# Kernel tuning notes

Hardware: AMD Instinct MI355X
Metric: run time of the kernel (lower is better)

Reference implementation:

```python
import jax, jax.numpy as jnp
import numpy as np

B, S, DIM, DA = 64, 4096, 256, 64
NEG = -1e30

def setup_inputs() -> dict:
    key = jax.random.key(0)
    k1, k2, k3, k4 = jax.random.split(key, 4)
    h = jax.random.normal(k1, (B, S, DIM), dtype=jnp.float32)
    mask = jax.random.randint(k2, (B, S), 0, 2).astype(jnp.bool_)
    # xavier_uniform with gain=1.414 as in the torch module
    lim_a = 1.414 * np.sqrt(6.0 / (DIM + DA))
    lim_b = 1.414 * np.sqrt(6.0 / (DA + 1))
    a = jax.random.uniform(k3, (DIM, DA), minval=-lim_a, maxval=lim_a, dtype=jnp.float32)
    b = jax.random.uniform(k4, (DA, 1), minval=-lim_b, maxval=lim_b, dtype=jnp.float32)
    return {"h": h, "mask": mask, "a": a, "b": b}

def reference(h, mask, a, b):
    # e: (B, S) additive-attention logits
    e = jnp.einsum('bsk,ko->bs', jnp.tanh(jnp.einsum('bsd,dk->bsk', h, a)), b)
    e = e + mask.astype(e.dtype) * NEG  # True == padding -> -1e30
    attn = jax.nn.softmax(e, axis=1)    # softmax over seq dim
    # weighted sum over seq: (B, DIM)
    return jnp.einsum('bs,bsd->bd', attn, h)
```

## Files before the change

kernel.cpp:

```cpp
#include <hip/hip_runtime.h>
#include <hip/hip_bf16.h>

#define B_    64
#define S_    4096
#define DIM_  256
#define DA_   64
#define NEG_  (-1e30f)

typedef __attribute__((ext_vector_type(8))) short short8;
typedef __attribute__((ext_vector_type(4))) float float4v;

static __device__ inline unsigned short f2bf(float x) {
    union { float f; unsigned u; } v; v.f = x;
    unsigned r = v.u + 0x7fffu + ((v.u >> 16) & 1u);
    return (unsigned short)(r >> 16);
}

__global__ __launch_bounds__(256) void prep_kernel(
    const float* __restrict__ a, const void* __restrict__ mask,
    unsigned short* __restrict__ at_sw, int* __restrict__ flag)
{
    int idx = blockIdx.x * 256 + threadIdx.x;
    int j    = idx & 7;
    int lane = (idx >> 3) & 63;
    int kbnt = idx >> 9;
    int kb   = kbnt & 7;
    int nt   = kbnt >> 3;
    int d  = kb * 32 + (lane >> 4) * 8 + j;
    int kf = nt * 16 + (lane & 15);
    at_sw[idx] = f2bf(a[d * DA_ + kf]);

    if (blockIdx.x == 0) {
        __shared__ int anynz;
        if (threadIdx.x == 0) anynz = 0;
        __syncthreads();
        const unsigned char* mb = (const unsigned char*)mask;
        int base = threadIdx.x * 4;
        int v = mb[base + 1] | mb[base + 2] | mb[base + 3];
        if (v) atomicOr(&anynz, 1);
        __syncthreads();
        if (threadIdx.x == 0) *flag = (anynz == 0) ? 1 : 0;
    }
}

__global__ __launch_bounds__(256) void logits_kernel(
    const float* __restrict__ h, const unsigned short* __restrict__ at_sw,
    const float* __restrict__ bvec, float* __restrict__ e,
    unsigned short* __restrict__ h16)
{
    __shared__ unsigned short hs[64 * 264];
    const int t = threadIdx.x;
    const long long s0 = (long long)blockIdx.x * 64;
    const float* hblk = h + s0 * DIM_;
    unsigned short* h16blk = h16 + s0 * DIM_;

    #pragma unroll
    for (int j = 0; j < 8; ++j) {
        int f2 = t + j * 256;
        int row = f2 >> 5;
        int col = (f2 & 31) * 8;
        const float* src = hblk + row * DIM_ + col;
        float4 v0 = *(const float4*)(src);
        float4 v1 = *(const float4*)(src + 4);
        uint2 p0, p1;
        p0.x = f2bf(v0.x) | ((unsigned)f2bf(v0.y) << 16);
        p0.y = f2bf(v0.z) | ((unsigned)f2bf(v0.w) << 16);
        p1.x = f2bf(v1.x) | ((unsigned)f2bf(v1.y) << 16);
        p1.y = f2bf(v1.z) | ((unsigned)f2bf(v1.w) << 16);
        *(uint2*)&hs[row * 264 + col]     = p0;
        *(uint2*)&hs[row * 264 + col + 4] = p1;
        union { _Float16 hh[8]; uint4 u; } pk;
        pk.hh[0] = (_Float16)v0.x; pk.hh[1] = (_Float16)v0.y;
        pk.hh[2] = (_Float16)v0.z; pk.hh[3] = (_Float16)v0.w;
        pk.hh[4] = (_Float16)v1.x; pk.hh[5] = (_Float16)v1.y;
        pk.hh[6] = (_Float16)v1.z; pk.hh[7] = (_Float16)v1.w;
        *(uint4*)(h16blk + (size_t)f2 * 8) = pk.u;
    }
    __syncthreads();

    const int wave = t >> 6;
    const int lane = t & 63;
    const int quad = lane >> 4;
    const int nrow = lane & 15;

    float4v acc[4];
    #pragma unroll
    for (int nt = 0; nt < 4; ++nt) acc[nt] = (float4v){0.f, 0.f, 0.f, 0.f};

    const unsigned short* hrow = &hs[(wave * 16 + nrow) * 264];
    #pragma unroll
    for (int kb = 0; kb < 8; ++kb) {
        short8 afrag = *(const short8*)(hrow + kb * 32 + quad * 8);
        #pragma unroll
        for (int nt = 0; nt < 4; ++nt) {
            short8 bfrag = *(const short8*)(at_sw + ((nt * 8 + kb) * 64 + lane) * 8);
            acc[nt] = __builtin_amdgcn_mfma_f32_16x16x32_bf16(afrag, bfrag, acc[nt], 0, 0, 0);
        }
    }

    float bv[4];
    #pragma unroll
    for (int nt = 0; nt < 4; ++nt) bv[nt] = bvec[nt * 16 + nrow];

    #pragma unroll
    for (int r = 0; r < 4; ++r) {
        float p = 0.f;
        #pragma unroll
        for (int nt = 0; nt < 4; ++nt) p += tanhf(acc[nt][r]) * bv[nt];
        p += __shfl_xor(p, 1);
        p += __shfl_xor(p, 2);
        p += __shfl_xor(p, 4);
        p += __shfl_xor(p, 8);
        if (nrow == r)
            e[s0 + wave * 16 + quad * 4 + r] = p;
    }
}

__global__ __launch_bounds__(1024) void softmax_kernel(
    float* __restrict__ e, const void* __restrict__ mask, const int* __restrict__ flag)
{
    const int b = blockIdx.x;
    const int t = threadIdx.x;
    const bool int32enc = (*flag != 0);
    const long long base = (long long)b * S_;

    float ev[4];
    #pragma unroll
    for (int i = 0; i < 4; ++i) {
        int s = t + i * 1024;
        float x = e[base + s];
        int m;
        if (int32enc) m = ((const int*)mask)[base + s];
        else          m = ((const unsigned char*)mask)[base + s];
        ev[i] = m ? NEG_ : x;
    }

    __shared__ float red[16];
    float mx = fmaxf(fmaxf(ev[0], ev[1]), fmaxf(ev[2], ev[3]));
    #pragma unroll
    for (int off = 32; off >= 1; off >>= 1) mx = fmaxf(mx, __shfl_xor(mx, off));
    if ((t & 63) == 0) red[t >> 6] = mx;
    __syncthreads();
    float m = red[0];
    #pragma unroll
    for (int i = 1; i < 16; ++i) m = fmaxf(m, red[i]);
    __syncthreads();

    float ex[4];
    float l = 0.f;
    #pragma unroll
    for (int i = 0; i < 4; ++i) { ex[i] = __expf(ev[i] - m); l += ex[i]; }
    #pragma unroll
    for (int off = 32; off >= 1; off >>= 1) l += __shfl_xor(l, off);
    if ((t & 63) == 0) red[t >> 6] = l;
    __syncthreads();
    float lt = 0.f;
    #pragma unroll
    for (int i = 0; i < 16; ++i) lt += red[i];

    float inv = 1.0f / lt;
    #pragma unroll
    for (int i = 0; i < 4; ++i) e[base + t + i * 1024] = ex[i] * inv;
}

__global__ __launch_bounds__(256) void wsum_kernel(
    const unsigned short* __restrict__ h16, const float* __restrict__ w,
    float* __restrict__ out)
{
    const int b = blockIdx.x >> 3;
    const int c = blockIdx.x & 7;
    const int t = threadIdx.x;
    const int wv = t >> 6;
    const int col = (t & 63) * 4;

    __shared__ float wch[512];
    __shared__ float red[4 * 256];
    const int sbase = c * 512;
    wch[t]       = w[(long long)b * S_ + sbase + t];
    wch[t + 256] = w[(long long)b * S_ + sbase + t + 256];
    __syncthreads();

    const unsigned short* hb = h16 + ((long long)b * S_ + sbase) * DIM_;
    float a0 = 0.f, a1 = 0.f, a2 = 0.f, a3 = 0.f;
    #pragma unroll 4
    for (int i = 0; i < 128; ++i) {
        int s = i * 4 + wv;
        union { ushort4 u; _Float16 hh[4]; } pk;
        pk.u = *(const ushort4*)(hb + (size_t)s * DIM_ + col);
        float wt = wch[s];
        a0 = fmaf(wt, (float)pk.hh[0], a0);
        a1 = fmaf(wt, (float)pk.hh[1], a1);
        a2 = fmaf(wt, (float)pk.hh[2], a2);
        a3 = fmaf(wt, (float)pk.hh[3], a3);
    }
    red[wv * 256 + col + 0] = a0;
    red[wv * 256 + col + 1] = a1;
    red[wv * 256 + col + 2] = a2;
    red[wv * 256 + col + 3] = a3;
    __syncthreads();

    float sum = red[t] + red[256 + t] + red[512 + t] + red[768 + t];
    atomicAdd(&out[b * DIM_ + t], sum);
}

extern "C" void kernel_launch(void* const* d_in, const int* in_sizes, int n_in,
                              void* d_out, int out_size, void* d_ws, size_t ws_size,
                              hipStream_t stream) {
    const float* h    = (const float*)d_in[0];
    const void*  mask = d_in[1];
    const float* a    = (const float*)d_in[2];
    const float* bvec = (const float*)d_in[3];
    float* out = (float*)d_out;

    char* ws = (char*)d_ws;
    unsigned short* at_sw = (unsigned short*)ws;
    int* flag             = (int*)(ws + 32768);
    float* e              = (float*)(ws + 36864);
    unsigned short* h16   = (unsigned short*)(ws + 1085440);

    hipMemsetAsync(d_out, 0, (size_t)B_ * DIM_ * sizeof(float), stream);
    prep_kernel<<<64, 256, 0, stream>>>(a, mask, at_sw, flag);
    logits_kernel<<<(B_ * S_) / 64, 256, 0, stream>>>(h, at_sw, bvec, e, h16);
    softmax_kernel<<<B_, 1024, 0, stream>>>(e, mask, flag);
    wsum_kernel<<<B_ * 8, 256, 0, stream>>>(h16, e, out);
}
```

Before: 420.9 us.

## Fuse logits, online softmax and weighted sum into one chunked kernel

Replaces the separate logits, softmax and weighted-sum kernels with one kernel. Each block handles a 256-row chunk of one batch and keeps an online (flash-style) running max and sum, accumulating the weighted sum from the fp16 tile already held in shared memory. A small merge kernel then rescales and combines the per-chunk partials. This removes the fp16 copy of h written to and re-read from global memory, the logits round trip, the memset and the atomics. In exchange the grid drops to 1024 blocks with serialized tiles and no overlap between load and compute, and the MFMA now uses fp16 instead of bf16.

```diff
diff --git a/kernel.cpp b/kernel.cpp
--- a/kernel.cpp
+++ b/kernel.cpp
@@ -1,24 +1,23 @@
 #include <hip/hip_runtime.h>
 #include <hip/hip_bf16.h>
 
-#define B_    64
-#define S_    4096
-#define DIM_  256
-#define DA_   64
-#define NEG_  (-1e30f)
-
-typedef __attribute__((ext_vector_type(8))) short short8;
-typedef __attribute__((ext_vector_type(4))) float float4v;
-
-static __device__ inline unsigned short f2bf(float x) {
-    union { float f; unsigned u; } v; v.f = x;
-    unsigned r = v.u + 0x7fffu + ((v.u >> 16) & 1u);
-    return (unsigned short)(r >> 16);
-}
+#define B_      64
+#define S_      4096
+#define DIM_    256
+#define DA_     64
+#define NEG_    (-1e30f)
+#define CHUNKS_ 16
+#define ROWS_   256
+#define TILES_  4
+#define LDH_    264
+#define PSTR_   258
+
+typedef _Float16 half8 __attribute__((ext_vector_type(8)));
+typedef float float4v __attribute__((ext_vector_type(4)));
 
 __global__ __launch_bounds__(256) void prep_kernel(
     const float* __restrict__ a, const void* __restrict__ mask,
-    unsigned short* __restrict__ at_sw, int* __restrict__ flag)
+    _Float16* __restrict__ at_sw, int* __restrict__ flag)
 {
     int idx = blockIdx.x * 256 + threadIdx.x;
     int j    = idx & 7;
@@ -28,7 +27,7 @@
     int nt   = kbnt >> 3;
     int d  = kb * 32 + (lane >> 4) * 8 + j;
     int kf = nt * 16 + (lane & 15);
-    at_sw[idx] = f2bf(a[d * DA_ + kf]);
+    at_sw[idx] = (_Float16)a[d * DA_ + kf];
 
     if (blockIdx.x == 0) {
         __shared__ int anynz;
@@ -43,164 +42,149 @@
     }
 }
 
-__global__ __launch_bounds__(256) void logits_kernel(
-    const float* __restrict__ h, const unsigned short* __restrict__ at_sw,
-    const float* __restrict__ bvec, float* __restrict__ e,
-    unsigned short* __restrict__ h16)
+__global__ __launch_bounds__(256) void fused_kernel(
+    const float* __restrict__ h, const _Float16* __restrict__ at_sw,
+    const float* __restrict__ bvec, const void* __restrict__ mask,
+    const int* __restrict__ flag, float* __restrict__ part)
 {
-    __shared__ unsigned short hs[64 * 264];
+    __shared__ _Float16 hf[64 * LDH_];
+    __shared__ float e_l[64];
+    __shared__ float w_l[64];
+    __shared__ float red[4 * 256];
+    __shared__ float m_s, l_s, resc_s;
+
     const int t = threadIdx.x;
-    const long long s0 = (long long)blockIdx.x * 64;
-    const float* hblk = h + s0 * DIM_;
-    unsigned short* h16blk = h16 + s0 * DIM_;
-
-    #pragma unroll
-    for (int j = 0; j < 8; ++j) {
-        int f2 = t + j * 256;
-        int row = f2 >> 5;
-        int col = (f2 & 31) * 8;
-        const float* src = hblk + row * DIM_ + col;
-        float4 v0 = *(const float4*)(src);
-        float4 v1 = *(const float4*)(src + 4);
-        uint2 p0, p1;
-        p0.x = f2bf(v0.x) | ((unsigned)f2bf(v0.y) << 16);
-        p0.y = f2bf(v0.z) | ((unsigned)f2bf(v0.w) << 16);
-        p1.x = f2bf(v1.x) | ((unsigned)f2bf(v1.y) << 16);
-        p1.y = f2bf(v1.z) | ((unsigned)f2bf(v1.w) << 16);
-        *(uint2*)&hs[row * 264 + col]     = p0;
-        *(uint2*)&hs[row * 264 + col + 4] = p1;
-        union { _Float16 hh[8]; uint4 u; } pk;
-        pk.hh[0] = (_Float16)v0.x; pk.hh[1] = (_Float16)v0.y;
-        pk.hh[2] = (_Float16)v0.z; pk.hh[3] = (_Float16)v0.w;
-        pk.hh[4] = (_Float16)v1.x; pk.hh[5] = (_Float16)v1.y;
-        pk.hh[6] = (_Float16)v1.z; pk.hh[7] = (_Float16)v1.w;
-        *(uint4*)(h16blk + (size_t)f2 * 8) = pk.u;
-    }
-    __syncthreads();
-
+    const int b = blockIdx.x >> 4;
+    const int c = blockIdx.x & (CHUNKS_ - 1);
     const int wave = t >> 6;
     const int lane = t & 63;
     const int quad = lane >> 4;
     const int nrow = lane & 15;
-
-    float4v acc[4];
-    #pragma unroll
-    for (int nt = 0; nt < 4; ++nt) acc[nt] = (float4v){0.f, 0.f, 0.f, 0.f};
-
-    const unsigned short* hrow = &hs[(wave * 16 + nrow) * 264];
-    #pragma unroll
-    for (int kb = 0; kb < 8; ++kb) {
-        short8 afrag = *(const short8*)(hrow + kb * 32 + quad * 8);
-        #pragma unroll
-        for (int nt = 0; nt < 4; ++nt) {
-            short8 bfrag = *(const short8*)(at_sw + ((nt * 8 + kb) * 64 + lane) * 8);
-            acc[nt] = __builtin_amdgcn_mfma_f32_16x16x32_bf16(afrag, bfrag, acc[nt], 0, 0, 0);
-        }
-    }
-
+    const bool int32enc = (*flag != 0);
+
+    if (t == 0) { m_s = NEG_; l_s = 0.f; }
+
+    const float* hb = h + ((long long)b * S_ + c * ROWS_) * DIM_;
     float bv[4];
     #pragma unroll
     for (int nt = 0; nt < 4; ++nt) bv[nt] = bvec[nt * 16 + nrow];
 
-    #pragma unroll
-    for (int r = 0; r < 4; ++r) {
-        float p = 0.f;
-        #pragma unroll
-        for (int nt = 0; nt < 4; ++nt) p += tanhf(acc[nt][r]) * bv[nt];
-        p += __shfl_xor(p, 1);
-        p += __shfl_xor(p, 2);
-        p += __shfl_xor(p, 4);
-        p += __shfl_xor(p, 8);
-        if (nrow == r)
-            e[s0 + wave * 16 + quad * 4 + r] = p;
+    const int dbase = (t & 63) * 4;
+    float acc0 = 0.f, acc1 = 0.f, acc2 = 0.f, acc3 = 0.f;
+
+    for (int tile = 0; tile < TILES_; ++tile) {
+        const float* hsrc = hb + (size_t)tile * 64 * DIM_;
+        #pragma unroll
+        for (int j = 0; j < 8; ++j) {
+            int f2 = t + j * 256;
+            int row = f2 >> 5;
+            int col = (f2 & 31) * 8;
+            const float* src = hsrc + row * DIM_ + col;
+            float4 v0 = *(const float4*)(src);
+            float4 v1 = *(const float4*)(src + 4);
+            union { _Float16 hh[8]; uint4 u; } pk;
+            pk.hh[0] = (_Float16)v0.x; pk.hh[1] = (_Float16)v0.y;
+            pk.hh[2] = (_Float16)v0.z; pk.hh[3] = (_Float16)v0.w;
+            pk.hh[4] = (_Float16)v1.x; pk.hh[5] = (_Float16)v1.y;
+            pk.hh[6] = (_Float16)v1.z; pk.hh[7] = (_Float16)v1.w;
+            *(uint4*)&hf[row * LDH_ + col] = pk.u;
+        }
+        __syncthreads();
+
+        float4v accm[4];
+        #pragma unroll
+        for (int nt = 0; nt < 4; ++nt) accm[nt] = (float4v){0.f, 0.f, 0.f, 0.f};
+        const _Float16* hrow = &hf[(wave * 16 + nrow) * LDH_];
+        #pragma unroll
+        for (int kb = 0; kb < 8; ++kb) {
+            half8 af = *(const half8*)(hrow + kb * 32 + quad * 8);
+            #pragma unroll
+            for (int nt = 0; nt < 4; ++nt) {
+                half8 bf = *(const half8*)(at_sw + ((nt * 8 + kb) * 64 + lane) * 8);
+                accm[nt] = __builtin_amdgcn_mfma_f32_16x16x32_f16(af, bf, accm[nt], 0, 0, 0);
+            }
+        }
+        #pragma unroll
+        for (int r = 0; r < 4; ++r) {
+            float p = 0.f;
+            #pragma unroll
+            for (int nt = 0; nt < 4; ++nt) p += tanhf(accm[nt][r]) * bv[nt];
+            p += __shfl_xor(p, 1);
+            p += __shfl_xor(p, 2);
+            p += __shfl_xor(p, 4);
+            p += __shfl_xor(p, 8);
+            if (nrow == r) e_l[wave * 16 + quad * 4 + r] = p;
+        }
+        __syncthreads();
+
+        if (wave == 0) {
+            long long mi = (long long)b * S_ + c * ROWS_ + tile * 64 + lane;
+            int mv = int32enc ? ((const int*)mask)[mi]
+                              : (int)((const unsigned char*)mask)[mi];
+            float ev = mv ? NEG_ : e_l[lane];
+            float mx = ev;
+            #pragma unroll
+            for (int off = 32; off >= 1; off >>= 1) mx = fmaxf(mx, __shfl_xor(mx, off));
+            float m_old = m_s;
+            float m_new = fmaxf(m_old, mx);
+            float wv_ = __expf(ev - m_new);
+            w_l[lane] = wv_;
+            float sm = wv_;
+            #pragma unroll
+            for (int off = 32; off >= 1; off >>= 1) sm += __shfl_xor(sm, off);
+            if (lane == 0) {
+                float rs = __expf(m_old - m_new);
+                l_s = l_s * rs + sm;
+                m_s = m_new;
+                resc_s = rs;
+            }
+        }
+        __syncthreads();
+
+        float rs = resc_s;
+        acc0 *= rs; acc1 *= rs; acc2 *= rs; acc3 *= rs;
+        #pragma unroll 4
+        for (int i = 0; i < 16; ++i) {
+            int s = i * 4 + wave;
+            float ws = w_l[s];
+            union { ushort4 u; _Float16 hh[4]; } pk;
+            pk.u = *(const ushort4*)((const unsigned short*)&hf[s * LDH_ + dbase]);
+            acc0 = fmaf(ws, (float)pk.hh[0], acc0);
+            acc1 = fmaf(ws, (float)pk.hh[1], acc1);
+            acc2 = fmaf(ws, (float)pk.hh[2], acc2);
+            acc3 = fmaf(ws, (float)pk.hh[3], acc3);
+        }
+        __syncthreads();
     }
-}
-
-__global__ __launch_bounds__(1024) void softmax_kernel(
-    float* __restrict__ e, const void* __restrict__ mask, const int* __restrict__ flag)
+
+    red[wave * 256 + dbase + 0] = acc0;
+    red[wave * 256 + dbase + 1] = acc1;
+    red[wave * 256 + dbase + 2] = acc2;
+    red[wave * 256 + dbase + 3] = acc3;
+    __syncthreads();
+    float sum = red[t] + red[256 + t] + red[512 + t] + red[768 + t];
+    float* pc = part + (size_t)(b * CHUNKS_ + c) * PSTR_;
+    pc[2 + t] = sum;
+    if (t == 0) { pc[0] = m_s; pc[1] = l_s; }
+}
+
+__global__ __launch_bounds__(256) void merge_kernel(
+    const float* __restrict__ part, float* __restrict__ out)
 {
     const int b = blockIdx.x;
     const int t = threadIdx.x;
-    const bool int32enc = (*flag != 0);
-    const long long base = (long long)b * S_;
-
-    float ev[4];
+    const float* pb = part + (size_t)b * CHUNKS_ * PSTR_;
+    float M = NEG_;
     #pragma unroll
-    for (int i = 0; i < 4; ++i) {
-        int s = t + i * 1024;
-        float x = e[base + s];
-        int m;
-        if (int32enc) m = ((const int*)mask)[base + s];
-        else          m = ((const unsigned char*)mask)[base + s];
-        ev[i] = m ? NEG_ : x;
+    for (int c = 0; c < CHUNKS_; ++c) M = fmaxf(M, pb[c * PSTR_]);
+    float L = 0.f, o = 0.f;
+    #pragma unroll
+    for (int c = 0; c < CHUNKS_; ++c) {
+        float sc = __expf(pb[c * PSTR_] - M);
+        L += pb[c * PSTR_ + 1] * sc;
+        o += pb[c * PSTR_ + 2 + t] * sc;
     }
-
-    __shared__ float red[16];
-    float mx = fmaxf(fmaxf(ev[0], ev[1]), fmaxf(ev[2], ev[3]));
-    #pragma unroll
-    for (int off = 32; off >= 1; off >>= 1) mx = fmaxf(mx, __shfl_xor(mx, off));
-    if ((t & 63) == 0) red[t >> 6] = mx;
-    __syncthreads();
-    float m = red[0];
-    #pragma unroll
-    for (int i = 1; i < 16; ++i) m = fmaxf(m, red[i]);
-    __syncthreads();
-
-    float ex[4];
-    float l = 0.f;
-    #pragma unroll
-    for (int i = 0; i < 4; ++i) { ex[i] = __expf(ev[i] - m); l += ex[i]; }
-    #pragma unroll
-    for (int off = 32; off >= 1; off >>= 1) l += __shfl_xor(l, off);
-    if ((t & 63) == 0) red[t >> 6] = l;
-    __syncthreads();
-    float lt = 0.f;
-    #pragma unroll
-    for (int i = 0; i < 16; ++i) lt += red[i];
-
-    float inv = 1.0f / lt;
-    #pragma unroll
-    for (int i = 0; i < 4; ++i) e[base + t + i * 1024] = ex[i] * inv;
-}
-
-__global__ __launch_bounds__(256) void wsum_kernel(
-    const unsigned short* __restrict__ h16, const float* __restrict__ w,
-    float* __restrict__ out)
-{
-    const int b = blockIdx.x >> 3;
-    const int c = blockIdx.x & 7;
-    const int t = threadIdx.x;
-    const int wv = t >> 6;
-    const int col = (t & 63) * 4;
-
-    __shared__ float wch[512];
-    __shared__ float red[4 * 256];
-    const int sbase = c * 512;
-    wch[t]       = w[(long long)b * S_ + sbase + t];
-    wch[t + 256] = w[(long long)b * S_ + sbase + t + 256];
-    __syncthreads();
-
-    const unsigned short* hb = h16 + ((long long)b * S_ + sbase) * DIM_;
-    float a0 = 0.f, a1 = 0.f, a2 = 0.f, a3 = 0.f;
-    #pragma unroll 4
-    for (int i = 0; i < 128; ++i) {
-        int s = i * 4 + wv;
-        union { ushort4 u; _Float16 hh[4]; } pk;
-        pk.u = *(const ushort4*)(hb + (size_t)s * DIM_ + col);
-        float wt = wch[s];
-        a0 = fmaf(wt, (float)pk.hh[0], a0);
-        a1 = fmaf(wt, (float)pk.hh[1], a1);
-        a2 = fmaf(wt, (float)pk.hh[2], a2);
-        a3 = fmaf(wt, (float)pk.hh[3], a3);
-    }
-    red[wv * 256 + col + 0] = a0;
-    red[wv * 256 + col + 1] = a1;
-    red[wv * 256 + col + 2] = a2;
-    red[wv * 256 + col + 3] = a3;
-    __syncthreads();
-
-    float sum = red[t] + red[256 + t] + red[512 + t] + red[768 + t];
-    atomicAdd(&out[b * DIM_ + t], sum);
+    out[b * DIM_ + t] = o / L;
 }
 
 extern "C" void kernel_launch(void* const* d_in, const int* in_sizes, int n_in,
@@ -213,14 +197,11 @@
     float* out = (float*)d_out;
 
     char* ws = (char*)d_ws;
-    unsigned short* at_sw = (unsigned short*)ws;
-    int* flag             = (int*)(ws + 32768);
-    float* e              = (float*)(ws + 36864);
-    unsigned short* h16   = (unsigned short*)(ws + 1085440);
-
-    hipMemsetAsync(d_out, 0, (size_t)B_ * DIM_ * sizeof(float), stream);
+    _Float16* at_sw = (_Float16*)ws;
+    int* flag       = (int*)(ws + 32768);
+    float* part     = (float*)(ws + 36864);
+
     prep_kernel<<<64, 256, 0, stream>>>(a, mask, at_sw, flag);
-    logits_kernel<<<(B_ * S_) / 64, 256, 0, stream>>>(h, at_sw, bvec, e, h16);
-    softmax_kernel<<<B_, 1024, 0, stream>>>(e, mask, flag);
-    wsum_kernel<<<B_ * 8, 256, 0, stream>>>(h16, e, out);
-}
+    fused_kernel<<<B_ * CHUNKS_, 256, 0, stream>>>(h, at_sw, bvec, mask, flag, part);
+    merge_kernel<<<B_, 256, 0, stream>>>(part, out);
+}
```

After: 377.2 us (median of 2 runs). -10.4%, faster.
